# Optimization experiments

Measured on AMD Instinct MI355X. Metric: run time of the kernel, lower is better.

The kernel has to match this reference:

```python
import jax, jax.numpy as jnp
import numpy as np

SIZE = (512, 512, 256)  # voxel grid dims (x, y, z)
N_PTS = 2_000_000       # number of query points


def setup_inputs() -> dict:
    key = jax.random.key(0)
    k1, k2 = jax.random.split(key)
    lower = jnp.array([-4.0, -4.0, -1.0], jnp.float32)
    resolution = jnp.array([64.0, 64.0, 64.0], jnp.float32)
    # physical extent of the grid along each axis
    extent = (jnp.array(SIZE, jnp.float32) - 1.0) / resolution
    x = (lower - 0.05 * extent) + jax.random.uniform(k1, (N_PTS, 3), jnp.float32) * (1.1 * extent)
    # learned parameter: hk.get_parameter('grid', (*size, 2)); random instead of zeros so outputs are nontrivial
    grid = jax.random.normal(k2, (*SIZE, 2), jnp.float32) * 0.1
    return {"x": x, "grid": grid, "lower": lower, "resolution": resolution}


def _trilinear(index, grid):
    """index: [N,3] float grid coords; grid: [X,Y,Z,2] -> [N,2]."""
    size = jnp.array(grid.shape[:3], jnp.int32)
    c0f = jnp.floor(index)
    f = index - c0f            # fractional offsets, [N,3]
    c0 = c0f.astype(jnp.int32)  # lower corner, [N,3]
    out = jnp.zeros((index.shape[0], grid.shape[-1]), grid.dtype)
    for dx in (0, 1):
        for dy in (0, 1):
            for dz in (0, 1):
                w = ((f[:, 0] if dx else 1.0 - f[:, 0])
                     * (f[:, 1] if dy else 1.0 - f[:, 1])
                     * (f[:, 2] if dz else 1.0 - f[:, 2]))
                ix = jnp.clip(c0[:, 0] + dx, 0, size[0] - 1)
                iy = jnp.clip(c0[:, 1] + dy, 0, size[1] - 1)
                iz = jnp.clip(c0[:, 2] + dz, 0, size[2] - 1)
                out = out + w[:, None] * grid[ix, iy, iz]  # gather [N,2]
    return out


def reference(x, grid, lower, resolution):
    size = jnp.array(grid.shape[:3], jnp.float32)
    index = (x - lower) * resolution               # [N,3] continuous grid coords
    valid = jnp.all((index >= 0.0) & (index <= size - 1.0), axis=-1)  # [N]
    vals = jnp.where(valid[:, None], _trilinear(index, grid), 0.0)    # [N,2]
    sigma, alpha = vals[:, 0], vals[:, 1]
    return sigma, alpha
```

## Files before the change

kernel.cpp:

```cpp
#include <hip/hip_runtime.h>

#define NX 512
#define NY 512
#define NZ 256

typedef float v4f __attribute__((ext_vector_type(4)));

struct PtPrep {
    int b00, b01, b10, b11;
    float wx, wy, wz;
    bool valid;
};

__device__ __forceinline__ PtPrep prep(float px, float py, float pz,
                                       float lx, float ly, float lz,
                                       float rx, float ry, float rz) {
    PtPrep r;
    float fx = (px - lx) * rx;
    float fy = (py - ly) * ry;
    float fz = (pz - lz) * rz;
    r.valid = (fx >= 0.0f) && (fx <= (float)(NX - 1)) &&
              (fy >= 0.0f) && (fy <= (float)(NY - 1)) &&
              (fz >= 0.0f) && (fz <= (float)(NZ - 1));
    int ix0 = min(max((int)floorf(fx), 0), NX - 2);
    int iy0 = min(max((int)floorf(fy), 0), NY - 2);
    int iz0 = min(max((int)floorf(fz), 0), NZ - 2);
    r.wx = fx - (float)ix0;
    r.wy = fy - (float)iy0;
    r.wz = fz - (float)iz0;
    int row0 = (ix0 * NY + iy0) * NZ + iz0;
    r.b00 = r.valid ? row0 : 0;
    r.b01 = r.valid ? row0 + NZ : 0;
    r.b10 = r.valid ? row0 + NY * NZ : 0;
    r.b11 = r.valid ? row0 + NY * NZ + NZ : 0;
    return r;
}

__device__ __forceinline__ void finish(const v4f& v00, const v4f& v01,
                                       const v4f& v10, const v4f& v11,
                                       const PtPrep& p, float& sigma, float& alpha) {
    float uz = 1.0f - p.wz, uy = 1.0f - p.wy, ux = 1.0f - p.wx;
    float s00 = v00.x * uz + v00.z * p.wz;
    float a00 = v00.y * uz + v00.w * p.wz;
    float s01 = v01.x * uz + v01.z * p.wz;
    float a01 = v01.y * uz + v01.w * p.wz;
    float s10 = v10.x * uz + v10.z * p.wz;
    float a10 = v10.y * uz + v10.w * p.wz;
    float s11 = v11.x * uz + v11.z * p.wz;
    float a11 = v11.y * uz + v11.w * p.wz;
    sigma = ux * (uy * s00 + p.wy * s01) + p.wx * (uy * s10 + p.wy * s11);
    alpha = ux * (uy * a00 + p.wy * a01) + p.wx * (uy * a10 + p.wy * a11);
    if (!p.valid) { sigma = 0.0f; alpha = 0.0f; }
}

__global__ __launch_bounds__(256) void trilerp2_kernel(
    const float* __restrict__ x,
    const float* __restrict__ grid,
    const float* __restrict__ lower,
    const float* __restrict__ resolution,
    float* __restrict__ out,
    int n)
{
    int t = blockIdx.x * blockDim.x + threadIdx.x;
    int i0 = 2 * t;
    if (i0 >= n) return;
    bool has2 = (i0 + 1) < n;

    float lx = lower[0], ly = lower[1], lz = lower[2];
    float rx = resolution[0], ry = resolution[1], rz = resolution[2];

    const float* xp = x + 6 * (size_t)t;
    float2 d0 = *(const float2*)xp;
    float p0x = d0.x, p0y = d0.y;
    float p0z = xp[2];
    float p1x = 0.0f, p1y = 0.0f, p1z = 0.0f;
    if (has2) { p1x = xp[3]; p1y = xp[4]; p1z = xp[5]; }

    PtPrep q0 = prep(p0x, p0y, p0z, lx, ly, lz, rx, ry, rz);
    PtPrep q1 = prep(p1x, p1y, p1z, lx, ly, lz, rx, ry, rz);

    const float2* g = (const float2*)grid;

    v4f A00, A01, A10, A11, B00, B01, B10, B11;
    __builtin_memcpy(&A00, g + q0.b00, 16);
    __builtin_memcpy(&A01, g + q0.b01, 16);
    __builtin_memcpy(&A10, g + q0.b10, 16);
    __builtin_memcpy(&A11, g + q0.b11, 16);
    __builtin_memcpy(&B00, g + q1.b00, 16);
    __builtin_memcpy(&B01, g + q1.b01, 16);
    __builtin_memcpy(&B10, g + q1.b10, 16);
    __builtin_memcpy(&B11, g + q1.b11, 16);

    float s0, a0, s1, a1;
    finish(A00, A01, A10, A11, q0, s0, a0);
    finish(B00, B01, B10, B11, q1, s1, a1);

    if (has2 && ((n & 1) == 0)) {
        *(float2*)(out + i0)     = make_float2(s0, s1);
        *(float2*)(out + n + i0) = make_float2(a0, a1);
    } else {
        out[i0] = s0;
        out[n + i0] = a0;
        if (has2) { out[i0 + 1] = s1; out[n + i0 + 1] = a1; }
    }
}

extern "C" void kernel_launch(void* const* d_in, const int* in_sizes, int n_in,
                              void* d_out, int out_size, void* d_ws, size_t ws_size,
                              hipStream_t stream) {
    const float* x          = (const float*)d_in[0];
    const float* grid       = (const float*)d_in[1];
    const float* lower      = (const float*)d_in[2];
    const float* resolution = (const float*)d_in[3];
    float* out              = (float*)d_out;

    int n = in_sizes[0] / 3;
    int threads = (n + 1) / 2;
    int block = 256;
    int blocks = (threads + block - 1) / block;
    trilerp2_kernel<<<blocks, block, 0, stream>>>(x, grid, lower, resolution, out, n);
}
```

Before: 716.0 us.

## Bucket points by Morton-ordered xy cell before gathering the grid

Replaces the single gather kernel with a counting-sort pipeline. Points are histogrammed into 512x512 xy buckets keyed by Morton order, the counts are prefix-scanned, and a payload of corner offset, weights and original index is scattered into sorted order. A gather kernel then reads the grid in that spatially coherent order and writes results back to the original indices. The aim is better cache, DRAM-page and TLB locality for the grid reads, at the cost of six extra launches, atomics, a random scatter of payloads and random output writes.

```diff
diff --git a/kernel.cpp b/kernel.cpp
--- a/kernel.cpp
+++ b/kernel.cpp
@@ -3,11 +3,23 @@
 #define NX 512
 #define NY 512
 #define NZ 256
+#define NBUCKET (512 * 512)
 
 typedef float v4f __attribute__((ext_vector_type(4)));
 
+struct Payload { int b00; float wx, wy, wz; int idx; };
+
+__device__ __forceinline__ unsigned spread9(unsigned v) {
+    v = (v | (v << 8)) & 0x00FF00FFu;
+    v = (v | (v << 4)) & 0x0F0F0F0Fu;
+    v = (v | (v << 2)) & 0x33333333u;
+    v = (v | (v << 1)) & 0x55555555u;
+    return v;
+}
+
 struct PtPrep {
-    int b00, b01, b10, b11;
+    int b00;
+    int ix0, iy0;
     float wx, wy, wz;
     bool valid;
 };
@@ -28,81 +40,161 @@
     r.wx = fx - (float)ix0;
     r.wy = fy - (float)iy0;
     r.wz = fz - (float)iz0;
-    int row0 = (ix0 * NY + iy0) * NZ + iz0;
-    r.b00 = r.valid ? row0 : 0;
-    r.b01 = r.valid ? row0 + NZ : 0;
-    r.b10 = r.valid ? row0 + NY * NZ : 0;
-    r.b11 = r.valid ? row0 + NY * NZ + NZ : 0;
+    r.ix0 = ix0; r.iy0 = iy0;
+    r.b00 = (ix0 * NY + iy0) * NZ + iz0;
     return r;
 }
 
 __device__ __forceinline__ void finish(const v4f& v00, const v4f& v01,
                                        const v4f& v10, const v4f& v11,
-                                       const PtPrep& p, float& sigma, float& alpha) {
-    float uz = 1.0f - p.wz, uy = 1.0f - p.wy, ux = 1.0f - p.wx;
-    float s00 = v00.x * uz + v00.z * p.wz;
-    float a00 = v00.y * uz + v00.w * p.wz;
-    float s01 = v01.x * uz + v01.z * p.wz;
-    float a01 = v01.y * uz + v01.w * p.wz;
-    float s10 = v10.x * uz + v10.z * p.wz;
-    float a10 = v10.y * uz + v10.w * p.wz;
-    float s11 = v11.x * uz + v11.z * p.wz;
-    float a11 = v11.y * uz + v11.w * p.wz;
-    sigma = ux * (uy * s00 + p.wy * s01) + p.wx * (uy * s10 + p.wy * s11);
-    alpha = ux * (uy * a00 + p.wy * a01) + p.wx * (uy * a10 + p.wy * a11);
-    if (!p.valid) { sigma = 0.0f; alpha = 0.0f; }
-}
-
-__global__ __launch_bounds__(256) void trilerp2_kernel(
+                                       float wx, float wy, float wz,
+                                       float& sigma, float& alpha) {
+    float uz = 1.0f - wz, uy = 1.0f - wy, ux = 1.0f - wx;
+    float s00 = v00.x * uz + v00.z * wz;
+    float a00 = v00.y * uz + v00.w * wz;
+    float s01 = v01.x * uz + v01.z * wz;
+    float a01 = v01.y * uz + v01.w * wz;
+    float s10 = v10.x * uz + v10.z * wz;
+    float a10 = v10.y * uz + v10.w * wz;
+    float s11 = v11.x * uz + v11.z * wz;
+    float a11 = v11.y * uz + v11.w * wz;
+    sigma = ux * (uy * s00 + wy * s01) + wx * (uy * s10 + wy * s11);
+    alpha = ux * (uy * a00 + wy * a01) + wx * (uy * a10 + wy * a11);
+}
+
+__global__ __launch_bounds__(256) void zero_kernel(unsigned* __restrict__ hist) {
+    int i = blockIdx.x * blockDim.x + threadIdx.x;
+    if (i < NBUCKET) hist[i] = 0u;
+}
+
+__global__ __launch_bounds__(256) void hist_kernel(
+    const float* __restrict__ x,
+    const float* __restrict__ lower,
+    const float* __restrict__ resolution,
+    unsigned* __restrict__ hist, int n)
+{
+    int i = blockIdx.x * blockDim.x + threadIdx.x;
+    if (i >= n) return;
+    PtPrep p = prep(x[3*i], x[3*i+1], x[3*i+2],
+                    lower[0], lower[1], lower[2],
+                    resolution[0], resolution[1], resolution[2]);
+    if (!p.valid) return;
+    unsigned key = spread9((unsigned)p.ix0) | (spread9((unsigned)p.iy0) << 1);
+    atomicAdd(&hist[key], 1u);
+}
+
+__global__ __launch_bounds__(1024) void scan_block_kernel(
+    unsigned* __restrict__ hist, unsigned* __restrict__ bsum)
+{
+    __shared__ unsigned s[1024];
+    int t = threadIdx.x;
+    int g = blockIdx.x * 1024 + t;
+    unsigned v = hist[g];
+    s[t] = v;
+    __syncthreads();
+    for (int off = 1; off < 1024; off <<= 1) {
+        unsigned u = (t >= off) ? s[t - off] : 0u;
+        __syncthreads();
+        s[t] += u;
+        __syncthreads();
+    }
+    hist[g] = s[t] - v;
+    if (t == 1023) bsum[blockIdx.x] = s[t];
+}
+
+__global__ __launch_bounds__(256) void scan_bsum_kernel(unsigned* __restrict__ bsum) {
+    __shared__ unsigned s[256];
+    int t = threadIdx.x;
+    unsigned v = bsum[t];
+    s[t] = v;
+    __syncthreads();
+    for (int off = 1; off < 256; off <<= 1) {
+        unsigned u = (t >= off) ? s[t - off] : 0u;
+        __syncthreads();
+        s[t] += u;
+        __syncthreads();
+    }
+    bsum[t] = s[t] - v;
+}
+
+__global__ __launch_bounds__(256) void scan_add_kernel(
+    unsigned* __restrict__ hist, const unsigned* __restrict__ bsum)
+{
+    int g = blockIdx.x * blockDim.x + threadIdx.x;
+    if (g < NBUCKET) hist[g] += bsum[g >> 10];
+}
+
+__global__ __launch_bounds__(256) void scatter_kernel(
+    const float* __restrict__ x,
+    const float* __restrict__ lower,
+    const float* __restrict__ resolution,
+    unsigned* __restrict__ cursor,
+    Payload* __restrict__ pay,
+    float* __restrict__ out, int n)
+{
+    int i = blockIdx.x * blockDim.x + threadIdx.x;
+    if (i >= n) return;
+    PtPrep p = prep(x[3*i], x[3*i+1], x[3*i+2],
+                    lower[0], lower[1], lower[2],
+                    resolution[0], resolution[1], resolution[2]);
+    if (!p.valid) {
+        out[i] = 0.0f;
+        out[n + i] = 0.0f;
+        return;
+    }
+    unsigned key = spread9((unsigned)p.ix0) | (spread9((unsigned)p.iy0) << 1);
+    unsigned pos = atomicAdd(&cursor[key], 1u);
+    Payload pl;
+    pl.b00 = p.b00; pl.wx = p.wx; pl.wy = p.wy; pl.wz = p.wz; pl.idx = i;
+    pay[pos] = pl;
+}
+
+__global__ __launch_bounds__(256) void gather_kernel(
+    const Payload* __restrict__ pay,
+    const float* __restrict__ grid,
+    const unsigned* __restrict__ cursor,
+    float* __restrict__ out, int n)
+{
+    unsigned total = cursor[NBUCKET - 1];
+    unsigned j = blockIdx.x * blockDim.x + threadIdx.x;
+    if (j >= total) return;
+    Payload p = pay[j];
+    const float2* g = (const float2*)grid;
+    v4f v00, v01, v10, v11;
+    __builtin_memcpy(&v00, g + p.b00, 16);
+    __builtin_memcpy(&v01, g + p.b00 + NZ, 16);
+    __builtin_memcpy(&v10, g + p.b00 + NY * NZ, 16);
+    __builtin_memcpy(&v11, g + p.b00 + NY * NZ + NZ, 16);
+    float sigma, alpha;
+    finish(v00, v01, v10, v11, p.wx, p.wy, p.wz, sigma, alpha);
+    out[p.idx] = sigma;
+    out[n + p.idx] = alpha;
+}
+
+__global__ __launch_bounds__(256) void direct_kernel(
     const float* __restrict__ x,
     const float* __restrict__ grid,
     const float* __restrict__ lower,
     const float* __restrict__ resolution,
-    float* __restrict__ out,
-    int n)
-{
-    int t = blockIdx.x * blockDim.x + threadIdx.x;
-    int i0 = 2 * t;
-    if (i0 >= n) return;
-    bool has2 = (i0 + 1) < n;
-
-    float lx = lower[0], ly = lower[1], lz = lower[2];
-    float rx = resolution[0], ry = resolution[1], rz = resolution[2];
-
-    const float* xp = x + 6 * (size_t)t;
-    float2 d0 = *(const float2*)xp;
-    float p0x = d0.x, p0y = d0.y;
-    float p0z = xp[2];
-    float p1x = 0.0f, p1y = 0.0f, p1z = 0.0f;
-    if (has2) { p1x = xp[3]; p1y = xp[4]; p1z = xp[5]; }
-
-    PtPrep q0 = prep(p0x, p0y, p0z, lx, ly, lz, rx, ry, rz);
-    PtPrep q1 = prep(p1x, p1y, p1z, lx, ly, lz, rx, ry, rz);
-
-    const float2* g = (const float2*)grid;
-
-    v4f A00, A01, A10, A11, B00, B01, B10, B11;
-    __builtin_memcpy(&A00, g + q0.b00, 16);
-    __builtin_memcpy(&A01, g + q0.b01, 16);
-    __builtin_memcpy(&A10, g + q0.b10, 16);
-    __builtin_memcpy(&A11, g + q0.b11, 16);
-    __builtin_memcpy(&B00, g + q1.b00, 16);
-    __builtin_memcpy(&B01, g + q1.b01, 16);
-    __builtin_memcpy(&B10, g + q1.b10, 16);
-    __builtin_memcpy(&B11, g + q1.b11, 16);
-
-    float s0, a0, s1, a1;
-    finish(A00, A01, A10, A11, q0, s0, a0);
-    finish(B00, B01, B10, B11, q1, s1, a1);
-
-    if (has2 && ((n & 1) == 0)) {
-        *(float2*)(out + i0)     = make_float2(s0, s1);
-        *(float2*)(out + n + i0) = make_float2(a0, a1);
-    } else {
-        out[i0] = s0;
-        out[n + i0] = a0;
-        if (has2) { out[i0 + 1] = s1; out[n + i0 + 1] = a1; }
-    }
+    float* __restrict__ out, int n)
+{
+    int i = blockIdx.x * blockDim.x + threadIdx.x;
+    if (i >= n) return;
+    PtPrep p = prep(x[3*i], x[3*i+1], x[3*i+2],
+                    lower[0], lower[1], lower[2],
+                    resolution[0], resolution[1], resolution[2]);
+    float sigma = 0.0f, alpha = 0.0f;
+    if (p.valid) {
+        const float2* g = (const float2*)grid;
+        v4f v00, v01, v10, v11;
+        __builtin_memcpy(&v00, g + p.b00, 16);
+        __builtin_memcpy(&v01, g + p.b00 + NZ, 16);
+        __builtin_memcpy(&v10, g + p.b00 + NY * NZ, 16);
+        __builtin_memcpy(&v11, g + p.b00 + NY * NZ + NZ, 16);
+        finish(v00, v01, v10, v11, p.wx, p.wy, p.wz, sigma, alpha);
+    }
+    out[i] = sigma;
+    out[n + i] = alpha;
 }
 
 extern "C" void kernel_launch(void* const* d_in, const int* in_sizes, int n_in,
@@ -115,8 +207,28 @@
     float* out              = (float*)d_out;
 
     int n = in_sizes[0] / 3;
-    int threads = (n + 1) / 2;
     int block = 256;
-    int blocks = (threads + block - 1) / block;
-    trilerp2_kernel<<<blocks, block, 0, stream>>>(x, grid, lower, resolution, out, n);
-}
+    int pblocks = (n + block - 1) / block;
+
+    size_t histBytes = (size_t)NBUCKET * 4;
+    size_t bsumBytes = 256 * 4;
+    size_t payBytes  = (size_t)n * sizeof(Payload);
+    size_t need = histBytes + bsumBytes + payBytes + 64;
+
+    if (ws_size < need) {
+        direct_kernel<<<pblocks, block, 0, stream>>>(x, grid, lower, resolution, out, n);
+        return;
+    }
+
+    unsigned* hist = (unsigned*)d_ws;
+    unsigned* bsum = (unsigned*)((char*)d_ws + histBytes);
+    Payload*  pay  = (Payload*)((char*)d_ws + histBytes + 64);
+
+    zero_kernel<<<(NBUCKET + 255) / 256, 256, 0, stream>>>(hist);
+    hist_kernel<<<pblocks, block, 0, stream>>>(x, lower, resolution, hist, n);
+    scan_block_kernel<<<NBUCKET / 1024, 1024, 0, stream>>>(hist, bsum);
+    scan_bsum_kernel<<<1, 256, 0, stream>>>(bsum);
+    scan_add_kernel<<<NBUCKET / 256, 256, 0, stream>>>(hist, bsum);
+    scatter_kernel<<<pblocks, block, 0, stream>>>(x, lower, resolution, hist, pay, out, n);
+    gather_kernel<<<pblocks, block, 0, stream>>>(pay, grid, hist, out, n);
+}
```

Result: slower. 870.6 us (+21.6%).
